# Kernel optimization log

Measured on AMD Instinct MI355X. Metric: run time of the kernel, lower is better.

The kernel has to match this reference:

```python
import jax, jax.numpy as jnp
import numpy as np

N_NODES = 50000
N_EDGES = 200000
D = 128
LN_EPS = 1e-5


def _layer_norm(x, g, b):
    mu = jnp.mean(x, axis=-1, keepdims=True)
    var = jnp.mean(jnp.square(x - mu), axis=-1, keepdims=True)
    return (x - mu) * jax.lax.rsqrt(var + LN_EPS) * g + b


def _mlp(x, W1, b1, W2, b2, W3, b3, g, beta):
    # 2 hidden ReLU layers + linear output + LayerNorm (MeshGraphNets style)
    h = jax.nn.relu(x @ W1 + b1)
    h = jax.nn.relu(h @ W2 + b2)
    h = h @ W3 + b3
    return _layer_norm(h, g, beta)


def setup_inputs() -> dict:
    key = jax.random.key(0)
    ks = jax.random.split(key, 12)
    d = {}
    d["node_features"] = jax.random.normal(ks[0], (N_NODES, D), dtype=jnp.float32)
    d["edge_features"] = jax.random.normal(ks[1], (N_EDGES, D), dtype=jnp.float32)
    d["senders"] = jax.random.randint(ks[2], (N_EDGES,), 0, N_NODES, dtype=jnp.int32)
    d["receivers"] = jax.random.randint(ks[3], (N_EDGES,), 0, N_NODES, dtype=jnp.int32)
    def lin(k, fan_in, fan_out):
        return jax.random.normal(k, (fan_in, fan_out), dtype=jnp.float32) / np.sqrt(fan_in)
    # edge MLP: [3D] -> D -> D -> D
    d["We1"] = lin(ks[4], 3 * D, D); d["be1"] = jnp.zeros((D,), jnp.float32)
    d["We2"] = lin(ks[5], D, D);     d["be2"] = jnp.zeros((D,), jnp.float32)
    d["We3"] = lin(ks[6], D, D);     d["be3"] = jnp.zeros((D,), jnp.float32)
    d["ge"] = jnp.ones((D,), jnp.float32); d["bege"] = jnp.zeros((D,), jnp.float32)
    # node MLP: [2D] -> D -> D -> D
    d["Wn1"] = lin(ks[7], 2 * D, D); d["bn1"] = jnp.zeros((D,), jnp.float32)
    d["Wn2"] = lin(ks[8], D, D);     d["bn2"] = jnp.zeros((D,), jnp.float32)
    d["Wn3"] = lin(ks[9], D, D);     d["bn3"] = jnp.zeros((D,), jnp.float32)
    d["gn"] = jnp.ones((D,), jnp.float32); d["begn"] = jnp.zeros((D,), jnp.float32)
    return d


def reference(node_features, edge_features, senders, receivers,
              We1, be1, We2, be2, We3, be3, ge, bege,
              Wn1, bn1, Wn2, bn2, Wn3, bn3, gn, begn):
    num_nodes = node_features.shape[0]
    # --- edge update: gather sender/receiver feats, concat, edge MLP ---
    edge_in = jnp.concatenate(
        [node_features[senders], node_features[receivers], edge_features], axis=-1)  # [E, 3D]
    new_edge = _mlp(edge_in, We1, be1, We2, be2, We3, be3, ge, bege)  # [E, D]
    # --- node update: scatter-sum aggregate, concat, node MLP ---
    agg = jax.ops.segment_sum(new_edge, receivers, num_segments=num_nodes)  # [N, D]
    node_in = jnp.concatenate([node_features, agg], axis=-1)  # [N, 2D]
    new_node = _mlp(node_in, Wn1, bn1, Wn2, bn2, Wn3, bn3, gn, begn)
    # --- residuals ---
    new_node = new_node + node_features
    new_edge = new_edge + edge_features
    return new_node, new_edge
```

## Files before the change

kernel.cpp:

```cpp
#include <hip/hip_runtime.h>

#define NNODES 50000
#define NEDGES 200000
#define DD 128
#define LN_EPS 1e-5f
#define NTH 256

typedef __attribute__((ext_vector_type(8))) short bf16x8;
typedef __attribute__((ext_vector_type(4))) float f32x4;
typedef __attribute__((ext_vector_type(16))) float f32x16;

template<int N> struct ic { static constexpr int value = N; };

__device__ __forceinline__ unsigned short bfr(float f) {
    union { float f; unsigned u; } v; v.f = f;
    return (unsigned short)((v.u + 0x7fffu + ((v.u >> 16) & 1u)) >> 16);
}

__global__ void build_wimg(const float* __restrict__ We1, const float* __restrict__ We2,
                           const float* __restrict__ We3, const float* __restrict__ Wn1,
                           const float* __restrict__ Wn2, const float* __restrict__ Wn3,
                           char* __restrict__ img_e, char* __restrict__ img_n) {
    int tid = blockIdx.x * NTH + threadIdx.x;
    const float* W; char* dst; int q;
    if      (tid <  6144) { W = We1; dst = img_e;             q = tid;         }
    else if (tid <  8192) { W = We2; dst = img_e + 12 * 8192; q = tid - 6144;  }
    else if (tid < 10240) { W = We3; dst = img_e + 16 * 8192; q = tid - 8192;  }
    else if (tid < 14336) { W = Wn1; dst = img_n;             q = tid - 10240; }
    else if (tid < 16384) { W = Wn2; dst = img_n + 8 * 8192;  q = tid - 14336; }
    else if (tid < 18432) { W = Wn3; dst = img_n + 12 * 8192; q = tid - 16384; }
    else return;
    int c = q >> 9, rem = q & 511;
    int nt = rem >> 7, r2 = rem & 127, ks = r2 >> 5, n32 = r2 & 31;
    int n = nt * 32 + n32;
    int k0 = c * 32 + ks * 8;
    unsigned short o[8];
    #pragma unroll
    for (int e = 0; e < 8; ++e)
        o[e] = bfr(W[(size_t)(k0 + e) * DD + n]);
    uint4 val;
    val.x = (unsigned)o[0] | ((unsigned)o[1] << 16);
    val.y = (unsigned)o[2] | ((unsigned)o[3] << 16);
    val.z = (unsigned)o[4] | ((unsigned)o[5] << 16);
    val.w = (unsigned)o[6] | ((unsigned)o[7] << 16);
    *(uint4*)(dst + (size_t)c * 8192 + nt * 2048 + ks * 512 + n32 * 16) = val;
}

__global__ __launch_bounds__(NTH)
void cvt_histo(const float* __restrict__ nodef, const int* __restrict__ recv,
               uint4* __restrict__ nodb, int* __restrict__ cnt) {
    const int tid0 = blockIdx.x * NTH + threadIdx.x;
    if (tid0 < NEDGES) atomicAdd(&cnt[recv[tid0]], 1);
    const int NG = NNODES * 16;
    for (int g = tid0; g < NG; g += gridDim.x * NTH) {
        f32x4 a = ((const f32x4*)nodef)[g * 2];
        f32x4 b = ((const f32x4*)nodef)[g * 2 + 1];
        uint4 o;
        o.x = (unsigned)bfr(a[0]) | ((unsigned)bfr(a[1]) << 16);
        o.y = (unsigned)bfr(a[2]) | ((unsigned)bfr(a[3]) << 16);
        o.z = (unsigned)bfr(b[0]) | ((unsigned)bfr(b[1]) << 16);
        o.w = (unsigned)bfr(b[2]) | ((unsigned)bfr(b[3]) << 16);
        nodb[g] = o;
    }
}

__global__ __launch_bounds__(NTH)
void csr_scan1(const int* __restrict__ cnt, int* __restrict__ part) {
    __shared__ int red[NTH];
    const int b = blockIdx.x, t = threadIdx.x;
    const int base = b * 196;
    int s = 0;
    for (int i = t; i < 196; i += NTH) {
        int idx = base + i;
        if (idx < NNODES) s += cnt[idx];
    }
    red[t] = s;
    __syncthreads();
    for (int d = NTH / 2; d > 0; d >>= 1) {
        if (t < d) red[t] += red[t + d];
        __syncthreads();
    }
    if (t == 0) part[b] = red[0];
}

__global__ __launch_bounds__(NTH)
void csr_scan2(const int* __restrict__ cnt, const int* __restrict__ part,
               int* __restrict__ off, int* __restrict__ cursor) {
    __shared__ int sp[NTH];
    const int t = threadIdx.x;
    sp[t] = part[t];
    __syncthreads();
    for (int d = 1; d < NTH; d <<= 1) {
        int v = (t >= d) ? sp[t - d] : 0;
        __syncthreads();
        sp[t] += v;
        __syncthreads();
    }
    int run = (t == 0) ? 0 : sp[t - 1];
    const int base = t * 196;
    for (int i = 0; i < 196; ++i) {
        int idx = base + i;
        if (idx < NNODES) { off[idx] = run; cursor[idx] = run; run += cnt[idx]; }
    }
    if (t == NTH - 1) off[NNODES] = NEDGES;
}

__global__ void csr_fill(const int* __restrict__ recv, int* __restrict__ cursor,
                         int* __restrict__ elist) {
    int e = blockIdx.x * NTH + threadIdx.x;
    if (e < NEDGES) {
        int p = atomicAdd(&cursor[recv[e]], 1);
        elist[p] = e;
    }
}

__global__ __launch_bounds__(NTH)
void aggregate(const unsigned* __restrict__ ybuf,
               const int* __restrict__ off, const int* __restrict__ elist,
               unsigned* __restrict__ aggb) {
    const int n = blockIdx.x * 4 + (threadIdx.x >> 6);
    const int l = threadIdx.x & 63;
    if (n >= NNODES) return;
    const int j0 = off[n], j1 = off[n + 1];
    float sx = 0.f, sy = 0.f;
    int j = j0;
    for (; j + 4 <= j1; j += 4) {
        const int e0 = elist[j], e1 = elist[j + 1], e2 = elist[j + 2], e3 = elist[j + 3];
        unsigned v0 = ybuf[(size_t)e0 * 64 + l];
        unsigned v1 = ybuf[(size_t)e1 * 64 + l];
        unsigned v2 = ybuf[(size_t)e2 * 64 + l];
        unsigned v3 = ybuf[(size_t)e3 * 64 + l];
        sx += __uint_as_float(v0 << 16) + __uint_as_float(v1 << 16)
            + __uint_as_float(v2 << 16) + __uint_as_float(v3 << 16);
        sy += __uint_as_float(v0 & 0xffff0000u) + __uint_as_float(v1 & 0xffff0000u)
            + __uint_as_float(v2 & 0xffff0000u) + __uint_as_float(v3 & 0xffff0000u);
    }
    for (; j < j1; ++j) {
        unsigned v = ybuf[(size_t)elist[j] * 64 + l];
        sx += __uint_as_float(v << 16);
        sy += __uint_as_float(v & 0xffff0000u);
    }
    aggb[(size_t)n * 64 + l] = (unsigned)bfr(sx) | ((unsigned)bfr(sy) << 16);
}

template<int MODE>
__global__ __launch_bounds__(NTH, 2)
void mgn_mfma(const float* __restrict__ nodef, const float* __restrict__ edgef,
              const unsigned short* __restrict__ nodb,
              const int* __restrict__ senders, const int* __restrict__ receivers,
              const char* __restrict__ img,
              const float* __restrict__ b1, const float* __restrict__ b2,
              const float* __restrict__ b3,
              const float* __restrict__ gamma, const float* __restrict__ beta,
              const unsigned short* __restrict__ aggb, unsigned* __restrict__ ybuf,
              float* __restrict__ outp)
{
    __shared__ char Hb[4 * 8192];

    const int t  = threadIdx.x;
    const int w  = t >> 6;
    const int l  = t & 63;
    const int ln = l & 31;
    const int hi = l >> 5;
    const int row0 = blockIdx.x * 128;
    const int gm = row0 + w * 32 + ln;
    constexpr int NROWS = (MODE == 0) ? NEDGES : NNODES;
    constexpr int NK1   = (MODE == 0) ? 12 : 8;
    constexpr int NCH   = NK1 + 8;
    const int gmc = gm < NROWS ? gm : NROWS - 1;
    const int sxH = ln & 15;

    int srow = 0, rrow = 0;
    if (MODE == 0) { srow = senders[gmc]; rrow = receivers[gmc]; }

    const f32x16 fz = {0.f,0.f,0.f,0.f,0.f,0.f,0.f,0.f,
                       0.f,0.f,0.f,0.f,0.f,0.f,0.f,0.f};
    f32x16 acc[4];
    #pragma unroll
    for (int nt = 0; nt < 4; ++nt) acc[nt] = fz;

    bf16x8 aS[3][4];
    bf16x8 bS[6][2];
    f32x4  fS[2][4];

    auto loadA = [&](int h, bf16x8* dst) {
        const char* p = img + (size_t)(h >> 1) * 8192
                      + (size_t)(((h & 1) * 2 + hi) * 512) + ln * 16;
        #pragma unroll
        for (int nt = 0; nt < 4; ++nt)
            dst[nt] = *(const bf16x8*)(p + nt * 2048);
    };

    auto loadBB = [&](auto CC, bf16x8* dst) {
        constexpr int c = decltype(CC)::value;
        const unsigned short* base;
        if constexpr (MODE == 0) {
            base = (c < 4) ? nodb + (size_t)srow * DD : nodb + (size_t)rrow * DD;
        } else {
            base = (c < 4) ? nodb + (size_t)gmc * DD : aggb + (size_t)gmc * DD;
        }
        const char* p = (const char*)base + (c & 3) * 64 + hi * 16;
        dst[0] = *(const bf16x8*)p;
        dst[1] = *(const bf16x8*)(p + 32);
    };

    auto loadBF = [&](auto CC, f32x4* dst) {
        constexpr int c = decltype(CC)::value;
        const float* p = edgef + (size_t)gmc * DD + (c & 3) * 32 + hi * 8;
        dst[0] = *(const f32x4*)p;
        dst[1] = *(const f32x4*)(p + 4);
        dst[2] = *(const f32x4*)(p + 16);
        dst[3] = *(const f32x4*)(p + 20);
    };

    auto cvtB = [&](const f32x4* br) {
        bf16x8 r;
        #pragma unroll
        for (int i = 0; i < 4; ++i) r[i]     = (short)bfr(br[0][i]);
        #pragma unroll
        for (int i = 0; i < 4; ++i) r[4 + i] = (short)bfr(br[1][i]);
        return r;
    };

    auto loadBH = [&](int ks, int kh) {
        const char* p = Hb + w * 8192 + ln * 256
                      + (((ks * 4 + kh * 2 + hi) ^ sxH) << 4);
        return *(const bf16x8*)p;
    };

    auto getB = [&](auto CC, int kh) -> bf16x8 {
        constexpr int c = decltype(CC)::value;
        if constexpr (c >= NK1) {
            return loadBH((c - NK1) & 3, kh);
        } else if constexpr (MODE == 0 && c >= 8) {
            return cvtB(&fS[c & 1][kh * 2]);
        } else {
            return bS[c % 6][kh];
        }
    };

    auto epiH = [&](const float* bias) {
        #pragma unroll
        for (int nt = 0; nt < 4; ++nt) {
            #pragma unroll
            for (int rq = 0; rq < 4; ++rq) {
                f32x4 bv = *(const f32x4*)(bias + nt * 32 + rq * 8 + hi * 4);
                unsigned short h[4];
                #pragma unroll
                for (int j = 0; j < 4; ++j)
                    h[j] = bfr(fmaxf(acc[nt][rq * 4 + j] + bv[j], 0.f));
                char* p = Hb + w * 8192 + ln * 256
                        + (((nt * 4 + rq) ^ sxH) << 4) + hi * 8;
                unsigned lo = (unsigned)h[0] | ((unsigned)h[1] << 16);
                unsigned hx = (unsigned)h[2] | ((unsigned)h[3] << 16);
                *(unsigned long long*)p =
                    (unsigned long long)lo | ((unsigned long long)hx << 32);
            }
            acc[nt] = fz;
        }
    };

    auto chunkfn = [&](auto CC) {
        constexpr int c = decltype(CC)::value;
        constexpr int h0 = 2 * c, h1 = 2 * c + 1;
        if constexpr (h0 + 2 < 2 * NCH) loadA(h0 + 2, aS[(h0 + 2) % 3]);
        {
            bf16x8 b0 = getB(CC, 0);
            #pragma unroll
            for (int nt = 0; nt < 4; ++nt)
                acc[nt] = __builtin_amdgcn_mfma_f32_32x32x16_bf16(
                    aS[h0 % 3][nt], b0, acc[nt], 0, 0, 0);
        }
        if constexpr (h1 + 2 < 2 * NCH) loadA(h1 + 2, aS[(h1 + 2) % 3]);
        {
            bf16x8 b1 = getB(CC, 1);
            #pragma unroll
            for (int nt = 0; nt < 4; ++nt)
                acc[nt] = __builtin_amdgcn_mfma_f32_32x32x16_bf16(
                    aS[h1 % 3][nt], b1, acc[nt], 0, 0, 0);
        }
        if constexpr (c + 6 < 8) loadBB(ic<c + 6>{}, bS[(c + 6) % 6]);
        if constexpr (MODE == 0 && c >= 6 && c <= 9) loadBF(ic<c + 2>{}, fS[(c + 2) & 1]);
    };

    loadBB(ic<0>{}, bS[0]); loadBB(ic<1>{}, bS[1]); loadBB(ic<2>{}, bS[2]);
    loadBB(ic<3>{}, bS[3]); loadBB(ic<4>{}, bS[4]); loadBB(ic<5>{}, bS[5]);
    loadA(0, aS[0]); loadA(1, aS[1]);

#define CH(C)                                                                \
    if constexpr ((C) < NCH) {                                               \
        chunkfn(ic<(C)>{});                                                  \
        if constexpr ((C) == NK1 - 1) epiH(b1);                              \
        if constexpr ((C) == NK1 + 3) epiH(b2);                              \
    }
    CH(0)  CH(1)  CH(2)  CH(3)  CH(4)  CH(5)  CH(6)  CH(7)
    CH(8)  CH(9)  CH(10) CH(11) CH(12) CH(13) CH(14) CH(15)
    CH(16) CH(17) CH(18) CH(19)
#undef CH

    float vsum = 0.f, vsq = 0.f;
    #pragma unroll
    for (int nt = 0; nt < 4; ++nt) {
        #pragma unroll
        for (int rq = 0; rq < 4; ++rq) {
            f32x4 bv = *(const f32x4*)(b3 + nt * 32 + rq * 8 + hi * 4);
            #pragma unroll
            for (int j = 0; j < 4; ++j) {
                float v = acc[nt][rq * 4 + j] + bv[j];
                acc[nt][rq * 4 + j] = v;
                vsum += v; vsq += v * v;
            }
        }
    }
    vsum += __shfl_xor(vsum, 32);
    vsq  += __shfl_xor(vsq, 32);
    const float mu = vsum * (1.f / DD);
    const float rs = rsqrtf(vsq * (1.f / DD) - mu * mu + LN_EPS);

    if (gm < NROWS) {
        const float* resid = ((MODE == 0) ? edgef : nodef) + (size_t)gm * DD;
        #pragma unroll
        for (int nt = 0; nt < 4; ++nt) {
            #pragma unroll
            for (int rq = 0; rq < 4; ++rq) {
                const int n0 = nt * 32 + rq * 8 + hi * 4;
                f32x4 gv = *(const f32x4*)(gamma + n0);
                f32x4 bv = *(const f32x4*)(beta + n0);
                f32x4 rv = *(const f32x4*)(resid + n0);
                float y[4];
                f32x4 o;
                #pragma unroll
                for (int j = 0; j < 4; ++j) {
                    y[j] = (acc[nt][rq * 4 + j] - mu) * rs * gv[j] + bv[j];
                    o[j] = y[j] + rv[j];
                }
                *(f32x4*)(outp + (size_t)gm * DD + n0) = o;
                if (MODE == 0) {
                    unsigned lo = (unsigned)bfr(y[0]) | ((unsigned)bfr(y[1]) << 16);
                    unsigned hx = (unsigned)bfr(y[2]) | ((unsigned)bfr(y[3]) << 16);
                    *(unsigned long long*)((char*)ybuf + (size_t)gm * 256 + n0 * 2) =
                        (unsigned long long)lo | ((unsigned long long)hx << 32);
                }
            }
        }
    }
}

extern "C" void kernel_launch(void* const* d_in, const int* in_sizes, int n_in,
                              void* d_out, int out_size, void* d_ws, size_t ws_size,
                              hipStream_t stream) {
    const float* nodef = (const float*)d_in[0];
    const float* edgef = (const float*)d_in[1];
    const int* senders   = (const int*)d_in[2];
    const int* receivers = (const int*)d_in[3];
    const float* We1 = (const float*)d_in[4],  *be1 = (const float*)d_in[5];
    const float* We2 = (const float*)d_in[6],  *be2 = (const float*)d_in[7];
    const float* We3 = (const float*)d_in[8],  *be3 = (const float*)d_in[9];
    const float* ge  = (const float*)d_in[10], *bege = (const float*)d_in[11];
    const float* Wn1 = (const float*)d_in[12], *bn1 = (const float*)d_in[13];
    const float* Wn2 = (const float*)d_in[14], *bn2 = (const float*)d_in[15];
    const float* Wn3 = (const float*)d_in[16], *bn3 = (const float*)d_in[17];
    const float* gn  = (const float*)d_in[18], *begn = (const float*)d_in[19];

    float* out_node = (float*)d_out;
    float* out_edge = (float*)d_out + (size_t)NNODES * DD;

    char* ws = (char*)d_ws;
    size_t o = 0;
    unsigned short* aggb = (unsigned short*)(ws + o); o += (size_t)NNODES * 256;
    unsigned* ybuf = (unsigned*)(ws + o);             o += (size_t)NEDGES * 256;
    unsigned short* nodb = (unsigned short*)(ws + o); o += (size_t)NNODES * 256;
    char* img_e = ws + o;           o += 20 * 8192;
    char* img_n = ws + o;           o += 16 * 8192;
    int* cnt    = (int*)(ws + o);   o += NNODES * 4;
    int* cursor = (int*)(ws + o);   o += NNODES * 4;
    int* off    = (int*)(ws + o);   o += (NNODES + 4) * 4;
    int* part   = (int*)(ws + o);   o += NTH * 4;
    int* elist  = (int*)(ws + o);   o += NEDGES * 4;

    hipMemsetAsync(cnt, 0, NNODES * 4, stream);
    cvt_histo<<<1024, NTH, 0, stream>>>(nodef, receivers, (uint4*)nodb, cnt);
    build_wimg<<<72, NTH, 0, stream>>>(We1, We2, We3, Wn1, Wn2, Wn3, img_e, img_n);
    csr_scan1<<<NTH, NTH, 0, stream>>>(cnt, part);
    csr_scan2<<<1, NTH, 0, stream>>>(cnt, part, off, cursor);
    csr_fill<<<(NEDGES + NTH - 1) / NTH, NTH, 0, stream>>>(receivers, cursor, elist);

    mgn_mfma<0><<<dim3((NEDGES + 127) / 128), dim3(NTH), 0, stream>>>(
        nodef, edgef, nodb, senders, receivers, img_e,
        be1, be2, be3, ge, bege, aggb, ybuf, out_edge);

    aggregate<<<(NNODES + 3) / 4, NTH, 0, stream>>>(ybuf, off, elist, (unsigned*)aggb);

    mgn_mfma<1><<<dim3((NNODES + 127) / 128), dim3(NTH), 0, stream>>>(
        nodef, edgef, nodb, senders, receivers, img_n,
        bn1, bn2, bn3, gn, begn, aggb, ybuf, out_node);
}
```

Baseline: 350.9 us.

## Stage MLP weights into LDS via async global_load_lds with swizzled layout

Weights were previously loaded from global memory straight into registers for every wave. They are now staged into a 5-slot LDS ring with global_load_lds, three chunks ahead, and the weight image is re-laid out with an XOR swizzle to avoid LDS bank conflicts. Operand prefetch depth is reduced to three buffers, and hand-tuned vmcnt waits plus block barriers order each chunk. This cuts redundant per-wave global weight traffic and register pressure. In exchange it adds 40KB of LDS, which may limit occupancy, and a barrier per chunk. The fixed vmcnt counts are fragile.

Result: faster. 321.3 us (-8.4%).

```diff
diff --git a/kernel.cpp b/kernel.cpp
--- a/kernel.cpp
+++ b/kernel.cpp
@@ -15,6 +15,14 @@
 __device__ __forceinline__ unsigned short bfr(float f) {
     union { float f; unsigned u; } v; v.f = f;
     return (unsigned short)((v.u + 0x7fffu + ((v.u >> 16) & 1u)) >> 16);
+}
+__device__ __forceinline__ unsigned pk2(float a, float b) {
+    return (unsigned)bfr(a) | ((unsigned)bfr(b) << 16);
+}
+__device__ __forceinline__ void gload_lds16(const void* g, void* l) {
+    __builtin_amdgcn_global_load_lds(
+        (const __attribute__((address_space(1))) void*)g,
+        (__attribute__((address_space(3))) void*)l, 16, 0, 0);
 }
 
 __global__ void build_wimg(const float* __restrict__ We1, const float* __restrict__ We2,
@@ -31,8 +39,9 @@
     else if (tid < 18432) { W = Wn3; dst = img_n + 12 * 8192; q = tid - 16384; }
     else return;
     int c = q >> 9, rem = q & 511;
-    int nt = rem >> 7, r2 = rem & 127, ks = r2 >> 5, n32 = r2 & 31;
+    int nt = rem >> 7, r2 = rem & 127, n32 = r2 >> 2, ks = r2 & 3;
     int n = nt * 32 + n32;
+    int sx = (n32 + (n32 >> 2)) & 3;
     int k0 = c * 32 + ks * 8;
     unsigned short o[8];
     #pragma unroll
@@ -43,7 +52,7 @@
     val.y = (unsigned)o[2] | ((unsigned)o[3] << 16);
     val.z = (unsigned)o[4] | ((unsigned)o[5] << 16);
     val.w = (unsigned)o[6] | ((unsigned)o[7] << 16);
-    *(uint4*)(dst + (size_t)c * 8192 + nt * 2048 + ks * 512 + n32 * 16) = val;
+    *(uint4*)(dst + (size_t)c * 8192 + nt * 2048 + n32 * 64 + ((ks ^ sx) << 4)) = val;
 }
 
 __global__ __launch_bounds__(NTH)
@@ -56,10 +65,8 @@
         f32x4 a = ((const f32x4*)nodef)[g * 2];
         f32x4 b = ((const f32x4*)nodef)[g * 2 + 1];
         uint4 o;
-        o.x = (unsigned)bfr(a[0]) | ((unsigned)bfr(a[1]) << 16);
-        o.y = (unsigned)bfr(a[2]) | ((unsigned)bfr(a[3]) << 16);
-        o.z = (unsigned)bfr(b[0]) | ((unsigned)bfr(b[1]) << 16);
-        o.w = (unsigned)bfr(b[2]) | ((unsigned)bfr(b[3]) << 16);
+        o.x = pk2(a[0], a[1]); o.y = pk2(a[2], a[3]);
+        o.z = pk2(b[0], b[1]); o.w = pk2(b[2], b[3]);
         nodb[g] = o;
     }
 }
@@ -125,11 +132,10 @@
     float sx = 0.f, sy = 0.f;
     int j = j0;
     for (; j + 4 <= j1; j += 4) {
-        const int e0 = elist[j], e1 = elist[j + 1], e2 = elist[j + 2], e3 = elist[j + 3];
-        unsigned v0 = ybuf[(size_t)e0 * 64 + l];
-        unsigned v1 = ybuf[(size_t)e1 * 64 + l];
-        unsigned v2 = ybuf[(size_t)e2 * 64 + l];
-        unsigned v3 = ybuf[(size_t)e3 * 64 + l];
+        unsigned v0 = ybuf[(size_t)elist[j] * 64 + l];
+        unsigned v1 = ybuf[(size_t)elist[j + 1] * 64 + l];
+        unsigned v2 = ybuf[(size_t)elist[j + 2] * 64 + l];
+        unsigned v3 = ybuf[(size_t)elist[j + 3] * 64 + l];
         sx += __uint_as_float(v0 << 16) + __uint_as_float(v1 << 16)
             + __uint_as_float(v2 << 16) + __uint_as_float(v3 << 16);
         sy += __uint_as_float(v0 & 0xffff0000u) + __uint_as_float(v1 & 0xffff0000u)
@@ -140,7 +146,7 @@
         sx += __uint_as_float(v << 16);
         sy += __uint_as_float(v & 0xffff0000u);
     }
-    aggb[(size_t)n * 64 + l] = (unsigned)bfr(sx) | ((unsigned)bfr(sy) << 16);
+    aggb[(size_t)n * 64 + l] = pk2(sx, sy);
 }
 
 template<int MODE>
@@ -155,6 +161,7 @@
               const unsigned short* __restrict__ aggb, unsigned* __restrict__ ybuf,
               float* __restrict__ outp)
 {
+    __shared__ char Wbuf[5 * 8192];
     __shared__ char Hb[4 * 8192];
 
     const int t  = threadIdx.x;
@@ -168,6 +175,7 @@
     constexpr int NK1   = (MODE == 0) ? 12 : 8;
     constexpr int NCH   = NK1 + 8;
     const int gmc = gm < NROWS ? gm : NROWS - 1;
+    const int sxA = (ln + (ln >> 2)) & 3;
     const int sxH = ln & 15;
 
     int srow = 0, rrow = 0;
@@ -179,16 +187,14 @@
     #pragma unroll
     for (int nt = 0; nt < 4; ++nt) acc[nt] = fz;
 
-    bf16x8 aS[3][4];
-    bf16x8 bS[6][2];
-    f32x4  fS[2][4];
-
-    auto loadA = [&](int h, bf16x8* dst) {
-        const char* p = img + (size_t)(h >> 1) * 8192
-                      + (size_t)(((h & 1) * 2 + hi) * 512) + ln * 16;
-        #pragma unroll
-        for (int nt = 0; nt < 4; ++nt)
-            dst[nt] = *(const bf16x8*)(p + nt * 2048);
+    bf16x8 bS[3][2];
+    f32x4  fS[3][4];
+
+    auto stageW = [&](int c) {
+        const char* src = img + (size_t)c * 8192 + t * 16;
+        char* dstl = Wbuf + (c % 5) * 8192 + t * 16;
+        gload_lds16(src, dstl);
+        gload_lds16(src + 4096, dstl + 4096);
     };
 
     auto loadBB = [&](auto CC, bf16x8* dst) {
@@ -214,12 +220,12 @@
     };
 
     auto cvtB = [&](const f32x4* br) {
-        bf16x8 r;
-        #pragma unroll
-        for (int i = 0; i < 4; ++i) r[i]     = (short)bfr(br[0][i]);
-        #pragma unroll
-        for (int i = 0; i < 4; ++i) r[4 + i] = (short)bfr(br[1][i]);
-        return r;
+        union { unsigned u[4]; bf16x8 v; } r;
+        r.u[0] = pk2(br[0][0], br[0][1]);
+        r.u[1] = pk2(br[0][2], br[0][3]);
+        r.u[2] = pk2(br[1][0], br[1][1]);
+        r.u[3] = pk2(br[1][2], br[1][3]);
+        return r.v;
     };
 
     auto loadBH = [&](int ks, int kh) {
@@ -233,9 +239,24 @@
         if constexpr (c >= NK1) {
             return loadBH((c - NK1) & 3, kh);
         } else if constexpr (MODE == 0 && c >= 8) {
-            return cvtB(&fS[c & 1][kh * 2]);
+            return cvtB(&fS[c % 3][kh * 2]);
         } else {
-            return bS[c % 6][kh];
+            return bS[c % 3][kh];
+        }
+    };
+
+    auto compute = [&](auto CC) {
+        constexpr int c = decltype(CC)::value;
+        const char* bp = Wbuf + (c % 5) * 8192 + ln * 64;
+        #pragma unroll
+        for (int kh = 0; kh < 2; ++kh) {
+            bf16x8 b = getB(CC, kh);
+            #pragma unroll
+            for (int nt = 0; nt < 4; ++nt) {
+                bf16x8 a = *(const bf16x8*)(bp + nt * 2048
+                            + (((kh * 2 + hi) ^ sxA) << 4));
+                acc[nt] = __builtin_amdgcn_mfma_f32_32x32x16_bf16(a, b, acc[nt], 0, 0, 0);
+            }
         }
     };
 
@@ -260,43 +281,52 @@
         }
     };
 
-    auto chunkfn = [&](auto CC) {
-        constexpr int c = decltype(CC)::value;
-        constexpr int h0 = 2 * c, h1 = 2 * c + 1;
-        if constexpr (h0 + 2 < 2 * NCH) loadA(h0 + 2, aS[(h0 + 2) % 3]);
-        {
-            bf16x8 b0 = getB(CC, 0);
-            #pragma unroll
-            for (int nt = 0; nt < 4; ++nt)
-                acc[nt] = __builtin_amdgcn_mfma_f32_32x32x16_bf16(
-                    aS[h0 % 3][nt], b0, acc[nt], 0, 0, 0);
-        }
-        if constexpr (h1 + 2 < 2 * NCH) loadA(h1 + 2, aS[(h1 + 2) % 3]);
-        {
-            bf16x8 b1 = getB(CC, 1);
-            #pragma unroll
-            for (int nt = 0; nt < 4; ++nt)
-                acc[nt] = __builtin_amdgcn_mfma_f32_32x32x16_bf16(
-                    aS[h1 % 3][nt], b1, acc[nt], 0, 0, 0);
-        }
-        if constexpr (c + 6 < 8) loadBB(ic<c + 6>{}, bS[(c + 6) % 6]);
-        if constexpr (MODE == 0 && c >= 6 && c <= 9) loadBF(ic<c + 2>{}, fS[(c + 2) & 1]);
-    };
-
-    loadBB(ic<0>{}, bS[0]); loadBB(ic<1>{}, bS[1]); loadBB(ic<2>{}, bS[2]);
-    loadBB(ic<3>{}, bS[3]); loadBB(ic<4>{}, bS[4]); loadBB(ic<5>{}, bS[5]);
-    loadA(0, aS[0]); loadA(1, aS[1]);
-
-#define CH(C)                                                                \
-    if constexpr ((C) < NCH) {                                               \
-        chunkfn(ic<(C)>{});                                                  \
-        if constexpr ((C) == NK1 - 1) epiH(b1);                              \
-        if constexpr ((C) == NK1 + 3) epiH(b2);                              \
-    }
-    CH(0)  CH(1)  CH(2)  CH(3)  CH(4)  CH(5)  CH(6)  CH(7)
-    CH(8)  CH(9)  CH(10) CH(11) CH(12) CH(13) CH(14) CH(15)
-    CH(16) CH(17) CH(18) CH(19)
-#undef CH
+#define PITER(C, VM)                                                          \
+    {                                                                         \
+        if constexpr ((C) + 3 < NCH) stageW((C) + 3);                         \
+        __builtin_amdgcn_sched_barrier(0);                                    \
+        if constexpr ((C) + 2 < NK1) {                                        \
+            if constexpr (MODE == 0 && (C) + 2 >= 8)                          \
+                loadBF(ic<(C) + 2>{}, fS[((C) + 2) % 3]);                     \
+            else                                                              \
+                loadBB(ic<(C) + 2>{}, bS[((C) + 2) % 3]);                     \
+        }                                                                     \
+        __builtin_amdgcn_sched_barrier(0);                                    \
+        asm volatile("s_waitcnt vmcnt(" #VM ")" ::: "memory");                \
+        __builtin_amdgcn_sched_barrier(0);                                    \
+        __builtin_amdgcn_s_barrier();                                         \
+        __builtin_amdgcn_sched_barrier(0);                                    \
+        compute(ic<(C)>{});                                                   \
+    }
+
+    stageW(0);
+    __builtin_amdgcn_sched_barrier(0);
+    loadBB(ic<0>{}, bS[0]);
+    __builtin_amdgcn_sched_barrier(0);
+    stageW(1);
+    __builtin_amdgcn_sched_barrier(0);
+    loadBB(ic<1>{}, bS[1]);
+    __builtin_amdgcn_sched_barrier(0);
+    stageW(2);
+    __builtin_amdgcn_sched_barrier(0);
+
+    if constexpr (MODE == 0) {
+        PITER(0, 10)  PITER(1, 10)  PITER(2, 10)  PITER(3, 12)
+        PITER(4, 12)  PITER(5, 12)  PITER(6, 14)  PITER(7, 16)
+        PITER(8, 18)  PITER(9, 20)  PITER(10, 16) PITER(11, 12)
+        epiH(b1);
+        PITER(12, 8)  PITER(13, 4)  PITER(14, 4)  PITER(15, 4)
+        epiH(b2);
+        PITER(16, 4)  PITER(17, 2)  PITER(18, 0)  PITER(19, 0)
+    } else {
+        PITER(0, 10)  PITER(1, 10)  PITER(2, 10)  PITER(3, 12)
+        PITER(4, 12)  PITER(5, 12)  PITER(6, 10)  PITER(7, 8)
+        epiH(b1);
+        PITER(8, 6)   PITER(9, 4)   PITER(10, 4)  PITER(11, 4)
+        epiH(b2);
+        PITER(12, 4)  PITER(13, 2)  PITER(14, 0)  PITER(15, 0)
+    }
+#undef PITER
 
     float vsum = 0.f, vsq = 0.f;
     #pragma unroll
@@ -336,10 +366,10 @@
                 }
                 *(f32x4*)(outp + (size_t)gm * DD + n0) = o;
                 if (MODE == 0) {
-                    unsigned lo = (unsigned)bfr(y[0]) | ((unsigned)bfr(y[1]) << 16);
-                    unsigned hx = (unsigned)bfr(y[2]) | ((unsigned)bfr(y[3]) << 16);
-                    *(unsigned long long*)((char*)ybuf + (size_t)gm * 256 + n0 * 2) =
-                        (unsigned long long)lo | ((unsigned long long)hx << 32);
+                    unsigned long long pkd =
+                        (unsigned long long)pk2(y[0], y[1])
+                      | ((unsigned long long)pk2(y[2], y[3]) << 32);
+                    *(unsigned long long*)((char*)ybuf + (size_t)gm * 256 + n0 * 2) = pkd;
                 }
             }
         }
```
